# Kernel optimization log

Measured on AMD Instinct MI355X. Metric: run time of the kernel, lower is better.

Reference implementation:

```python
import jax, jax.numpy as jnp
import numpy as np

HIDDEN = 128
INT_EMB = 64
NUM_SPH = 7
E = 262144
T = 2097152


def _glorot(key, shape):
    fan_in, fan_out = shape[1], shape[0]
    limit = np.sqrt(6.0 / (fan_in + fan_out))
    return jax.random.uniform(key, shape, jnp.float32, -limit, limit)


def setup_inputs() -> dict:
    key = jax.random.key(0)
    ks = jax.random.split(key, 10)
    edge_attr = jax.random.normal(ks[0], (E, HIDDEN), jnp.float32)
    sbf = jax.random.normal(ks[1], (T, NUM_SPH), jnp.float32)
    idx_kj = jax.random.randint(ks[2], (T,), 0, E)
    idx_ji = jax.random.randint(ks[3], (T,), 0, E)
    # Linear weights stored torch-style as [out_features, in_features]
    W_sbf0 = _glorot(ks[4], (NUM_SPH, NUM_SPH))
    W_sbf = _glorot(ks[5], (INT_EMB, NUM_SPH))
    W_e1 = _glorot(ks[6], (HIDDEN, 2 * HIDDEN))
    b_e1 = jnp.zeros((HIDDEN,), jnp.float32)
    W_down = _glorot(ks[7], (INT_EMB, HIDDEN))
    W_up = _glorot(ks[8], (HIDDEN, INT_EMB))
    return {
        "edge_attr": edge_attr, "sbf": sbf, "idx_kj": idx_kj, "idx_ji": idx_ji,
        "W_sbf0": W_sbf0, "W_sbf": W_sbf, "W_e1": W_e1, "b_e1": b_e1,
        "W_down": W_down, "W_up": W_up,
    }


def reference(edge_attr, sbf, idx_kj, idx_ji, W_sbf0, W_sbf, W_e1, b_e1, W_down, W_up):
    act = jax.nn.silu
    # x = act(lin_down(edge_attr))  [E, INT_EMB]
    x = act(edge_attr @ W_down.T)
    # sbf basis projections [T, INT_EMB]
    s = (sbf @ W_sbf0.T) @ W_sbf.T
    # gather by idx_kj, modulate, scatter-add onto idx_ji
    m = x[idx_kj] * s                                   # [T, INT_EMB]
    agg = jax.ops.segment_sum(m, idx_ji, num_segments=edge_attr.shape[0])
    # up-project and edge update
    u = act(agg @ W_up.T)                               # [E, HIDDEN]
    h = act(jnp.concatenate([edge_attr, u], axis=-1) @ W_e1.T + b_e1)
    return h + edge_attr
```

## Files before the change

### kernel.cpp

```cpp
#include <hip/hip_runtime.h>
#include <hip/hip_bf16.h>

#define NSPH 7

typedef short bf16x8 __attribute__((ext_vector_type(8)));
typedef float f32x4 __attribute__((ext_vector_type(4)));

static __device__ __forceinline__ ushort f2b(float f) {
    union { __hip_bfloat16 h; ushort u; } v; v.h = __float2bfloat16(f); return v.u;
}
static __device__ __forceinline__ float b2f(ushort u) {
    union { unsigned int i; float f; } v; v.i = ((unsigned int)u) << 16; return v.f;
}
static __device__ __forceinline__ float silu_f(float v) {
    return v / (1.0f + __expf(-v));
}
static __device__ __forceinline__ bf16x8 ld8_f32_to_bf16(const float* p) {
    float4 p0 = *(const float4*)p;
    float4 p1 = *(const float4*)(p + 4);
    bf16x8 r;
    r[0] = (short)f2b(p0.x); r[1] = (short)f2b(p0.y);
    r[2] = (short)f2b(p0.z); r[3] = (short)f2b(p0.w);
    r[4] = (short)f2b(p1.x); r[5] = (short)f2b(p1.y);
    r[6] = (short)f2b(p1.z); r[7] = (short)f2b(p1.w);
    return r;
}

__launch_bounds__(256)
__global__ void k1_down(const float* __restrict__ edge, const float* __restrict__ Wd,
                        ushort* __restrict__ X) {
    const int tid  = threadIdx.x;
    const int lane = tid & 63;
    const int w    = tid >> 6;
    const int quad = lane >> 4;
    const int m16  = lane & 15;
    const int r0   = blockIdx.x * 128 + w * 32;

    f32x4 acc[2][4];
#pragma unroll
    for (int mi = 0; mi < 2; mi++)
#pragma unroll
        for (int ni = 0; ni < 4; ni++) acc[mi][ni] = (f32x4){0.f, 0.f, 0.f, 0.f};

#pragma unroll
    for (int k = 0; k < 128; k += 32) {
        bf16x8 a[2], b[4];
#pragma unroll
        for (int mi = 0; mi < 2; mi++)
            a[mi] = ld8_f32_to_bf16(&edge[(size_t)(r0 + mi * 16 + m16) * 128 + k + quad * 8]);
#pragma unroll
        for (int ni = 0; ni < 4; ni++)
            b[ni] = ld8_f32_to_bf16(&Wd[(ni * 16 + m16) * 128 + k + quad * 8]);
#pragma unroll
        for (int mi = 0; mi < 2; mi++)
#pragma unroll
            for (int ni = 0; ni < 4; ni++)
                acc[mi][ni] = __builtin_amdgcn_mfma_f32_16x16x32_bf16(a[mi], b[ni], acc[mi][ni], 0, 0, 0);
    }
#pragma unroll
    for (int mi = 0; mi < 2; mi++)
#pragma unroll
        for (int ni = 0; ni < 4; ni++)
#pragma unroll
            for (int r = 0; r < 4; r++) {
                int row = r0 + mi * 16 + quad * 4 + r;
                int col = ni * 16 + m16;
                X[(size_t)row * 64 + col] = f2b(silu_f(acc[mi][ni][r]));
            }
}

__launch_bounds__(256)
__global__ void k_hist(const int* __restrict__ ji, int* __restrict__ counts, int T) {
    int i = blockIdx.x * 256 + threadIdx.x;
    int n = gridDim.x * 256;
    for (int t = i; t < T; t += n) atomicAdd(&counts[ji[t]], 1);
}

__launch_bounds__(256)
__global__ void k_scan_bsum(const int* __restrict__ counts, int* __restrict__ bsum) {
    __shared__ int sm[256];
    int tid = threadIdx.x;
    sm[tid] = counts[blockIdx.x * 256 + tid];
    __syncthreads();
#pragma unroll
    for (int off = 128; off > 0; off >>= 1) {
        if (tid < off) sm[tid] += sm[tid + off];
        __syncthreads();
    }
    if (tid == 0) bsum[blockIdx.x] = sm[0];
}

__launch_bounds__(1024)
__global__ void k_scan_top(int* __restrict__ bsum, int NB) {
    __shared__ int sm[1024];
    int tid = threadIdx.x;
    int v = (tid < NB) ? bsum[tid] : 0;
    sm[tid] = v;
    __syncthreads();
    for (int off = 1; off < 1024; off <<= 1) {
        int x = (tid >= off) ? sm[tid - off] : 0;
        __syncthreads();
        sm[tid] += x;
        __syncthreads();
    }
    if (tid < NB) bsum[tid] = sm[tid] - v;
}

__launch_bounds__(256)
__global__ void k_scan_down(const int* __restrict__ counts, const int* __restrict__ bsum,
                            int* __restrict__ offsets, int* __restrict__ cursor) {
    __shared__ int sm[256];
    int tid = threadIdx.x;
    int g = blockIdx.x * 256 + tid;
    int v = counts[g];
    sm[tid] = v;
    __syncthreads();
    for (int off = 1; off < 256; off <<= 1) {
        int x = (tid >= off) ? sm[tid - off] : 0;
        __syncthreads();
        sm[tid] += x;
        __syncthreads();
    }
    int o = bsum[blockIdx.x] + sm[tid] - v;
    offsets[g] = o;
    cursor[g]  = o;
}

__launch_bounds__(256)
__global__ void k_scatter_pay(const int* __restrict__ ji, const int* __restrict__ kj,
                              const float* __restrict__ sbf, int* __restrict__ cursor,
                              int* __restrict__ kj_s, float* __restrict__ out, int T) {
    int i = blockIdx.x * 256 + threadIdx.x;
    int n = gridDim.x * 256;
    for (int t = i; t < T; t += n) {
        int b = ji[t];
        int pos = atomicAdd(&cursor[b], 1);
        kj_s[pos] = kj[t];
        const float* sp = &sbf[(size_t)t * NSPH];
        float4 lo, hi;
        lo.x = sp[0]; lo.y = sp[1]; lo.z = sp[2]; lo.w = sp[3];
        hi.x = sp[4]; hi.y = sp[5]; hi.z = sp[6]; hi.w = 0.f;
        float* dst = &out[((size_t)(pos >> 3)) * 128 + 64 + (pos & 7) * 8];
        *(float4*)dst = lo;
        *(float4*)(dst + 4) = hi;
    }
}

__launch_bounds__(256)
__global__ void k2_sorted(const int* __restrict__ kj_s, const int* __restrict__ offsets,
                          const int* __restrict__ counts, const ushort* __restrict__ X,
                          const float* __restrict__ Wsbf, const float* __restrict__ Wsbf0,
                          float* __restrict__ out, int E) {
    const int lane = threadIdx.x & 63;
    float wj[NSPH], wc[NSPH];
#pragma unroll
    for (int i = 0; i < NSPH; i++) wj[i] = Wsbf[lane * NSPH + i];
#pragma unroll
    for (int k = 0; k < NSPH; k++) {
        float a = 0.f;
#pragma unroll
        for (int i = 0; i < NSPH; i++) a += wj[i] * Wsbf0[i * NSPH + k];
        wc[k] = a;
    }

    int gw = (blockIdx.x * 256 + threadIdx.x) >> 6;
    int nw = (gridDim.x * 256) >> 6;
    int segw = (E + nw - 1) / nw;
    int rbeg = gw * segw;
    int rend = rbeg + segw; if (rend > E) rend = E;

    for (int r = rbeg; r < rend; ++r) {
        int rs = __builtin_amdgcn_readfirstlane(r);
        int st = offsets[rs];
        int c  = counts[rs];
        float acc = 0.f;
        for (int done = 0; done < c; done += 64) {
            int cl = c - done; if (cl > 64) cl = 64;
            int j  = st + done + lane;
            int kjv = 0;
            float sb0 = 0.f, sb1 = 0.f, sb2 = 0.f, sb3 = 0.f, sb4 = 0.f, sb5 = 0.f, sb6 = 0.f;
            if (lane < cl) {
                kjv = kj_s[j];
                const float* sp = &out[((size_t)(j >> 3)) * 128 + 64 + (j & 7) * 8];
                float4 lo = *(const float4*)sp;
                float4 hi = *(const float4*)(sp + 4);
                sb0 = lo.x; sb1 = lo.y; sb2 = lo.z; sb3 = lo.w;
                sb4 = hi.x; sb5 = hi.y; sb6 = hi.z;
            }
            for (int i0 = 0; i0 < cl; i0 += 8) {
                int aa[8];
                ushort raw[8];
#pragma unroll
                for (int k8 = 0; k8 < 8; k8++) {
                    int ii = i0 + k8; if (ii > cl - 1) ii = cl - 1;
                    aa[k8] = __builtin_amdgcn_readlane(kjv, ii);
                    raw[k8] = X[(size_t)aa[k8] * 64 + lane];
                }
#pragma unroll
                for (int k8 = 0; k8 < 8; k8++) {
                    int ii = i0 + k8; if (ii > cl - 1) ii = cl - 1;
                    float s = wc[0] * __int_as_float(__builtin_amdgcn_readlane(__float_as_int(sb0), ii));
                    s += wc[1] * __int_as_float(__builtin_amdgcn_readlane(__float_as_int(sb1), ii));
                    s += wc[2] * __int_as_float(__builtin_amdgcn_readlane(__float_as_int(sb2), ii));
                    s += wc[3] * __int_as_float(__builtin_amdgcn_readlane(__float_as_int(sb3), ii));
                    s += wc[4] * __int_as_float(__builtin_amdgcn_readlane(__float_as_int(sb4), ii));
                    s += wc[5] * __int_as_float(__builtin_amdgcn_readlane(__float_as_int(sb5), ii));
                    s += wc[6] * __int_as_float(__builtin_amdgcn_readlane(__float_as_int(sb6), ii));
                    if (i0 + k8 >= cl) s = 0.f;
                    acc += b2f(raw[k8]) * s;
                }
            }
        }
        out[(size_t)rs * 128 + lane] = acc;
    }
}

__launch_bounds__(256)
__global__ void k3_fused(const float* __restrict__ edge, const float* __restrict__ Wu,
                         const float* __restrict__ We, const float* __restrict__ bias,
                         float* out) {
    __shared__ __align__(16) short Ut[128 * 136];
    const int tid  = threadIdx.x;
    const int lane = tid & 63;
    const int w    = tid >> 6;
    const int quad = lane >> 4;
    const int m16  = lane & 15;
    const int r0   = blockIdx.x * 128;
    const int rowbase = (w >> 1) * 64;
    const int colbase = (w & 1) * 64;

    f32x4 acc1[4][4];
#pragma unroll
    for (int mi = 0; mi < 4; mi++)
#pragma unroll
        for (int ni = 0; ni < 4; ni++) acc1[mi][ni] = (f32x4){0.f, 0.f, 0.f, 0.f};

#pragma unroll
    for (int kk = 0; kk < 64; kk += 32) {
        bf16x8 a[4], b[4];
#pragma unroll
        for (int mi = 0; mi < 4; mi++)
            a[mi] = ld8_f32_to_bf16(&out[(size_t)(r0 + rowbase + mi * 16 + m16) * 128 + kk + quad * 8]);
#pragma unroll
        for (int ni = 0; ni < 4; ni++)
            b[ni] = ld8_f32_to_bf16(&Wu[(colbase + ni * 16 + m16) * 64 + kk + quad * 8]);
#pragma unroll
        for (int mi = 0; mi < 4; mi++)
#pragma unroll
            for (int ni = 0; ni < 4; ni++)
                acc1[mi][ni] = __builtin_amdgcn_mfma_f32_16x16x32_bf16(a[mi], b[ni], acc1[mi][ni], 0, 0, 0);
    }
#pragma unroll
    for (int mi = 0; mi < 4; mi++)
#pragma unroll
        for (int ni = 0; ni < 4; ni++)
#pragma unroll
            for (int r = 0; r < 4; r++) {
                int rl = rowbase + mi * 16 + quad * 4 + r;
                int cl = colbase + ni * 16 + m16;
                Ut[rl * 136 + cl] = (short)f2b(silu_f(acc1[mi][ni][r]));
            }
    __syncthreads();

    f32x4 acc2[4][4];
#pragma unroll
    for (int mi = 0; mi < 4; mi++)
#pragma unroll
        for (int ni = 0; ni < 4; ni++) acc2[mi][ni] = (f32x4){0.f, 0.f, 0.f, 0.f};

#pragma unroll
    for (int k = 0; k < 256; k += 32) {
        bf16x8 a[4], b[4];
#pragma unroll
        for (int mi = 0; mi < 4; mi++) {
            int rl = rowbase + mi * 16 + m16;
            if (k < 128)
                a[mi] = ld8_f32_to_bf16(&edge[(size_t)(r0 + rl) * 128 + k + quad * 8]);
            else
                a[mi] = *(const bf16x8*)&Ut[rl * 136 + (k - 128) + quad * 8];
        }
#pragma unroll
        for (int ni = 0; ni < 4; ni++)
            b[ni] = ld8_f32_to_bf16(&We[(size_t)(colbase + ni * 16 + m16) * 256 + k + quad * 8]);
#pragma unroll
        for (int mi = 0; mi < 4; mi++)
#pragma unroll
            for (int ni = 0; ni < 4; ni++)
                acc2[mi][ni] = __builtin_amdgcn_mfma_f32_16x16x32_bf16(a[mi], b[ni], acc2[mi][ni], 0, 0, 0);
    }

#pragma unroll
    for (int mi = 0; mi < 4; mi++)
#pragma unroll
        for (int ni = 0; ni < 4; ni++) {
            int col = colbase + ni * 16 + m16;
            float bcol = bias[col];
#pragma unroll
            for (int r = 0; r < 4; r++) {
                int row = r0 + rowbase + mi * 16 + quad * 4 + r;
                float pre = acc2[mi][ni][r] + bcol;
                out[(size_t)row * 128 + col] = silu_f(pre) + edge[(size_t)row * 128 + col];
            }
        }
}

extern "C" void kernel_launch(void* const* d_in, const int* in_sizes, int n_in,
                              void* d_out, int out_size, void* d_ws, size_t ws_size,
                              hipStream_t stream) {
    const float* edge  = (const float*)d_in[0];
    const float* sbf   = (const float*)d_in[1];
    const int*   idxkj = (const int*)d_in[2];
    const int*   idxji = (const int*)d_in[3];
    const float* Wsbf0 = (const float*)d_in[4];
    const float* Wsbf  = (const float*)d_in[5];
    const float* We1   = (const float*)d_in[6];
    const float* be1   = (const float*)d_in[7];
    const float* Wdown = (const float*)d_in[8];
    const float* Wup   = (const float*)d_in[9];

    const int E = in_sizes[0] / 128;
    const int T = in_sizes[2];
    const int NB = E / 256;

    ushort* X       = (ushort*)d_ws;
    int*    counts  = (int*)((char*)d_ws + (size_t)E * 64 * 2);
    int*    offsets = counts + E;
    int*    cursor  = offsets + E;
    int*    kj_s    = cursor + E;
    int*    bsum    = kj_s + T;

    float* out = (float*)d_out;

    hipMemsetAsync(counts, 0, (size_t)E * sizeof(int), stream);

    k1_down<<<E / 128, 256, 0, stream>>>(edge, Wdown, X);

    k_hist<<<2048, 256, 0, stream>>>(idxji, counts, T);
    k_scan_bsum<<<NB, 256, 0, stream>>>(counts, bsum);
    k_scan_top<<<1, 1024, 0, stream>>>(bsum, NB);
    k_scan_down<<<NB, 256, 0, stream>>>(counts, bsum, offsets, cursor);
    k_scatter_pay<<<2048, 256, 0, stream>>>(idxji, idxkj, sbf, cursor, kj_s, out, T);

    k2_sorted<<<4096, 256, 0, stream>>>(kj_s, offsets, counts, X, Wsbf, Wsbf0, out, E);

    k3_fused<<<E / 128, 256, 0, stream>>>(edge, Wup, We1, be1, out);
}
```

Before: 874.3 us.

## Stage bf16 copies of edge, weights and aggregation for the fused edge-update GEMM

k1_down now writes a bf16 copy of edge_attr into the first half of each output row. A new kernel pre-converts W_e1 and W_up to bf16, and k2 stores the aggregation as a compact bf16 buffer instead of fp32 in the output. k3 reads these bf16 operands directly and uses 512 threads with 32-row tiles per wave, with a barrier before the final overwrite of out. The aim is to cut fp32 read traffic and per-load conversion in k3 and raise occupancy, at the cost of extra writes in k1 and one more small kernel launch.

```diff
diff --git a/kernel.cpp b/kernel.cpp
--- a/kernel.cpp
+++ b/kernel.cpp
@@ -28,7 +28,7 @@
 
 __launch_bounds__(256)
 __global__ void k1_down(const float* __restrict__ edge, const float* __restrict__ Wd,
-                        ushort* __restrict__ X) {
+                        ushort* __restrict__ X, ushort* __restrict__ outb) {
     const int tid  = threadIdx.x;
     const int lane = tid & 63;
     const int w    = tid >> 6;
@@ -46,8 +46,11 @@
     for (int k = 0; k < 128; k += 32) {
         bf16x8 a[2], b[4];
 #pragma unroll
-        for (int mi = 0; mi < 2; mi++)
-            a[mi] = ld8_f32_to_bf16(&edge[(size_t)(r0 + mi * 16 + m16) * 128 + k + quad * 8]);
+        for (int mi = 0; mi < 2; mi++) {
+            int row = r0 + mi * 16 + m16;
+            a[mi] = ld8_f32_to_bf16(&edge[(size_t)row * 128 + k + quad * 8]);
+            *(bf16x8*)&outb[(size_t)row * 256 + k + quad * 8] = a[mi];
+        }
 #pragma unroll
         for (int ni = 0; ni < 4; ni++)
             b[ni] = ld8_f32_to_bf16(&Wd[(ni * 16 + m16) * 128 + k + quad * 8]);
@@ -67,6 +70,14 @@
                 int col = ni * 16 + m16;
                 X[(size_t)row * 64 + col] = f2b(silu_f(acc[mi][ni][r]));
             }
+}
+
+__launch_bounds__(256)
+__global__ void k_cvt_w(const float* __restrict__ We, const float* __restrict__ Wu,
+                        ushort* __restrict__ Web, ushort* __restrict__ Wub) {
+    int i = blockIdx.x * 256 + threadIdx.x;
+    if (i < 128 * 256) Web[i] = f2b(We[i]);
+    if (i < 128 * 64)  Wub[i] = f2b(Wu[i]);
 }
 
 __launch_bounds__(256)
@@ -150,7 +161,7 @@
 __global__ void k2_sorted(const int* __restrict__ kj_s, const int* __restrict__ offsets,
                           const int* __restrict__ counts, const ushort* __restrict__ X,
                           const float* __restrict__ Wsbf, const float* __restrict__ Wsbf0,
-                          float* __restrict__ out, int E) {
+                          const float* __restrict__ out, ushort* __restrict__ aggb, int E) {
     const int lane = threadIdx.x & 63;
     float wj[NSPH], wc[NSPH];
 #pragma unroll
@@ -211,86 +222,90 @@
                 }
             }
         }
-        out[(size_t)rs * 128 + lane] = acc;
-    }
-}
-
-__launch_bounds__(256)
-__global__ void k3_fused(const float* __restrict__ edge, const float* __restrict__ Wu,
-                         const float* __restrict__ We, const float* __restrict__ bias,
-                         float* out) {
-    __shared__ __align__(16) short Ut[128 * 136];
+        aggb[(size_t)rs * 64 + lane] = f2b(acc);
+    }
+}
+
+__launch_bounds__(512)
+__global__ void k3_fused(const float* __restrict__ edge, const ushort* __restrict__ aggb,
+                         const ushort* __restrict__ Wub, const ushort* __restrict__ Web,
+                         const float* __restrict__ bias, float* __restrict__ out) {
+    __shared__ __align__(16) ushort Ut[128 * 136];
     const int tid  = threadIdx.x;
     const int lane = tid & 63;
     const int w    = tid >> 6;
     const int quad = lane >> 4;
     const int m16  = lane & 15;
+    const int wr   = w >> 1;
+    const int wc   = w & 1;
     const int r0   = blockIdx.x * 128;
-    const int rowbase = (w >> 1) * 64;
-    const int colbase = (w & 1) * 64;
-
-    f32x4 acc1[4][4];
-#pragma unroll
-    for (int mi = 0; mi < 4; mi++)
-#pragma unroll
-        for (int ni = 0; ni < 4; ni++) acc1[mi][ni] = (f32x4){0.f, 0.f, 0.f, 0.f};
+    const int rowbase = wr * 32;
+    const int colbase = wc * 64;
+    ushort* outb = (ushort*)out;
+
+    f32x4 acc[2][4];
+#pragma unroll
+    for (int mi = 0; mi < 2; mi++)
+#pragma unroll
+        for (int ni = 0; ni < 4; ni++) acc[mi][ni] = (f32x4){0.f, 0.f, 0.f, 0.f};
 
 #pragma unroll
     for (int kk = 0; kk < 64; kk += 32) {
-        bf16x8 a[4], b[4];
-#pragma unroll
-        for (int mi = 0; mi < 4; mi++)
-            a[mi] = ld8_f32_to_bf16(&out[(size_t)(r0 + rowbase + mi * 16 + m16) * 128 + kk + quad * 8]);
-#pragma unroll
-        for (int ni = 0; ni < 4; ni++)
-            b[ni] = ld8_f32_to_bf16(&Wu[(colbase + ni * 16 + m16) * 64 + kk + quad * 8]);
-#pragma unroll
-        for (int mi = 0; mi < 4; mi++)
+        bf16x8 a[2], b[4];
+#pragma unroll
+        for (int mi = 0; mi < 2; mi++)
+            a[mi] = *(const bf16x8*)&aggb[(size_t)(r0 + rowbase + mi * 16 + m16) * 64 + kk + quad * 8];
+#pragma unroll
+        for (int ni = 0; ni < 4; ni++)
+            b[ni] = *(const bf16x8*)&Wub[(colbase + ni * 16 + m16) * 64 + kk + quad * 8];
+#pragma unroll
+        for (int mi = 0; mi < 2; mi++)
 #pragma unroll
             for (int ni = 0; ni < 4; ni++)
-                acc1[mi][ni] = __builtin_amdgcn_mfma_f32_16x16x32_bf16(a[mi], b[ni], acc1[mi][ni], 0, 0, 0);
-    }
-#pragma unroll
-    for (int mi = 0; mi < 4; mi++)
+                acc[mi][ni] = __builtin_amdgcn_mfma_f32_16x16x32_bf16(a[mi], b[ni], acc[mi][ni], 0, 0, 0);
+    }
+#pragma unroll
+    for (int mi = 0; mi < 2; mi++)
 #pragma unroll
         for (int ni = 0; ni < 4; ni++)
 #pragma unroll
             for (int r = 0; r < 4; r++) {
                 int rl = rowbase + mi * 16 + quad * 4 + r;
                 int cl = colbase + ni * 16 + m16;
-                Ut[rl * 136 + cl] = (short)f2b(silu_f(acc1[mi][ni][r]));
-            }
-    __syncthreads();
-
-    f32x4 acc2[4][4];
-#pragma unroll
-    for (int mi = 0; mi < 4; mi++)
-#pragma unroll
-        for (int ni = 0; ni < 4; ni++) acc2[mi][ni] = (f32x4){0.f, 0.f, 0.f, 0.f};
+                Ut[rl * 136 + cl] = f2b(silu_f(acc[mi][ni][r]));
+            }
+    __syncthreads();
+
+#pragma unroll
+    for (int mi = 0; mi < 2; mi++)
+#pragma unroll
+        for (int ni = 0; ni < 4; ni++) acc[mi][ni] = (f32x4){0.f, 0.f, 0.f, 0.f};
 
 #pragma unroll
     for (int k = 0; k < 256; k += 32) {
-        bf16x8 a[4], b[4];
-#pragma unroll
-        for (int mi = 0; mi < 4; mi++) {
+        bf16x8 a[2], b[4];
+#pragma unroll
+        for (int mi = 0; mi < 2; mi++) {
             int rl = rowbase + mi * 16 + m16;
             if (k < 128)
-                a[mi] = ld8_f32_to_bf16(&edge[(size_t)(r0 + rl) * 128 + k + quad * 8]);
+                a[mi] = *(const bf16x8*)&outb[(size_t)(r0 + rl) * 256 + k + quad * 8];
             else
                 a[mi] = *(const bf16x8*)&Ut[rl * 136 + (k - 128) + quad * 8];
         }
 #pragma unroll
         for (int ni = 0; ni < 4; ni++)
-            b[ni] = ld8_f32_to_bf16(&We[(size_t)(colbase + ni * 16 + m16) * 256 + k + quad * 8]);
-#pragma unroll
-        for (int mi = 0; mi < 4; mi++)
+            b[ni] = *(const bf16x8*)&Web[(size_t)(colbase + ni * 16 + m16) * 256 + k + quad * 8];
+#pragma unroll
+        for (int mi = 0; mi < 2; mi++)
 #pragma unroll
             for (int ni = 0; ni < 4; ni++)
-                acc2[mi][ni] = __builtin_amdgcn_mfma_f32_16x16x32_bf16(a[mi], b[ni], acc2[mi][ni], 0, 0, 0);
-    }
-
-#pragma unroll
-    for (int mi = 0; mi < 4; mi++)
+                acc[mi][ni] = __builtin_amdgcn_mfma_f32_16x16x32_bf16(a[mi], b[ni], acc[mi][ni], 0, 0, 0);
+    }
+
+    __syncthreads();
+
+#pragma unroll
+    for (int mi = 0; mi < 2; mi++)
 #pragma unroll
         for (int ni = 0; ni < 4; ni++) {
             int col = colbase + ni * 16 + m16;
@@ -298,7 +313,7 @@
 #pragma unroll
             for (int r = 0; r < 4; r++) {
                 int row = r0 + rowbase + mi * 16 + quad * 4 + r;
-                float pre = acc2[mi][ni][r] + bcol;
+                float pre = acc[mi][ni][r] + bcol;
                 out[(size_t)row * 128 + col] = silu_f(pre) + edge[(size_t)row * 128 + col];
             }
         }
@@ -323,17 +338,21 @@
     const int NB = E / 256;
 
     ushort* X       = (ushort*)d_ws;
-    int*    counts  = (int*)((char*)d_ws + (size_t)E * 64 * 2);
+    ushort* aggb    = X + (size_t)E * 64;
+    int*    counts  = (int*)(aggb + (size_t)E * 64);
     int*    offsets = counts + E;
     int*    cursor  = offsets + E;
     int*    kj_s    = cursor + E;
     int*    bsum    = kj_s + T;
+    ushort* Web     = (ushort*)(bsum + 1024);
+    ushort* Wub     = Web + 128 * 256;
 
     float* out = (float*)d_out;
 
     hipMemsetAsync(counts, 0, (size_t)E * sizeof(int), stream);
 
-    k1_down<<<E / 128, 256, 0, stream>>>(edge, Wdown, X);
+    k_cvt_w<<<128, 256, 0, stream>>>(We1, Wup, Web, Wub);
+    k1_down<<<E / 128, 256, 0, stream>>>(edge, Wdown, X, (ushort*)out);
 
     k_hist<<<2048, 256, 0, stream>>>(idxji, counts, T);
     k_scan_bsum<<<NB, 256, 0, stream>>>(counts, bsum);
@@ -341,7 +360,8 @@
     k_scan_down<<<NB, 256, 0, stream>>>(counts, bsum, offsets, cursor);
     k_scatter_pay<<<2048, 256, 0, stream>>>(idxji, idxkj, sbf, cursor, kj_s, out, T);
 
-    k2_sorted<<<4096, 256, 0, stream>>>(kj_s, offsets, counts, X, Wsbf, Wsbf0, out, E);
-
-    k3_fused<<<E / 128, 256, 0, stream>>>(edge, Wup, We1, be1, out);
-}
+    k2_sorted<<<4096, 256, 0, stream>>>(kj_s, offsets, counts, X, Wsbf, Wsbf0,
+                                        out, aggb, E);
+
+    k3_fused<<<E / 128, 512, 0, stream>>>(edge, aggb, Wub, Web, be1, out);
+}
```

Result: faster. 805.1 us (-7.9%).
